# Optimization experiments

Hardware: AMD Instinct MI355X
Metric: run time of the kernel (lower is better)

The kernel has to match this reference:

```python
import jax, jax.numpy as jnp
import numpy as np

R, B, D, H, N, F = 8, 16, 32, 128, 2048, 256
HALF_LOG_2PI = np.float32(0.9189385332046727)  # 0.5*log(2*pi)


def _made_masks():
    # MADE masks for a 2-hidden-layer network (D -> H -> H -> 2*D), params=2,
    # input_order='random' per (region, batch) network, hidden degrees cyclic in [1, D-1].
    rng = np.random.RandomState(0)
    deg_in = np.stack([np.stack([rng.permutation(D) + 1 for _ in range(B)]) for _ in range(R)])  # [R,B,D]
    h_deg = (np.arange(H) % (D - 1)) + 1  # [H]
    M1 = (deg_in[:, :, :, None] <= h_deg[None, None, None, :]).astype(np.float32)  # [R,B,D,H]
    M2 = np.broadcast_to((h_deg[:, None] <= h_deg[None, :]).astype(np.float32), (R, B, H, H)).copy()  # [R,B,H,H]
    out_deg = np.repeat(deg_in, 2, axis=-1)  # [R,B,2D]; index k=2*d+p matches reshape(...,D,2)
    M3 = (h_deg[None, None, :, None] < out_deg[:, :, None, :]).astype(np.float32)  # [R,B,H,2D]
    return M1, M2, M3


def setup_inputs() -> dict:
    key = jax.random.key(0)
    k1, k2, k3, k4 = jax.random.split(key, 4)
    x = jax.random.normal(k1, (N, F), dtype=jnp.float32)
    W1 = jax.random.normal(k2, (R, B, D, H), dtype=jnp.float32) * 0.1
    W2 = jax.random.normal(k3, (R, B, H, H), dtype=jnp.float32) * 0.05
    W3 = jax.random.normal(k4, (R, B, H, 2 * D), dtype=jnp.float32) * 0.02
    M1, M2, M3 = _made_masks()
    region_idx = jnp.arange(F, dtype=jnp.int64 if jax.config.jax_enable_x64 else jnp.int32).reshape(R, D)
    return {"x": x, "W1": W1, "W2": W2, "W3": W3,
            "M1": jnp.asarray(M1), "M2": jnp.asarray(M2), "M3": jnp.asarray(M3),
            "region_idx": region_idx}


def reference(x, W1, W2, W3, M1, M2, M3, region_idx):
    # Gather per-region features: [N, R, D] -> [R, N, D]
    xr = jnp.transpose(x[:, region_idx], (1, 0, 2))
    # Masked MADE forward (no bias, relu), batched over all R*B networks.
    h1 = jax.nn.relu(jnp.einsum('rnd,rbdh->rbnh', xr, W1 * M1))
    h2 = jax.nn.relu(jnp.einsum('rbnh,rbhk->rbnk', h1, W2 * M2))
    out = jnp.einsum('rbnk,rbko->rbno', h2, W3 * M3)  # [R,B,N,2D]
    out = out.reshape(out.shape[0], out.shape[1], out.shape[2], -1, 2)  # [R,B,N,D,2]
    shift, log_scale = out[..., 0], out[..., 1]
    # MAF inverse (one pass): u = (y - shift) * exp(-log_scale);
    # log_prob = sum_d Normal(0,1).log_prob(u_d) - log_scale_d
    u = (xr[:, None] - shift) * jnp.exp(-log_scale)  # [R,B,N,D]
    ll = jnp.sum(-0.5 * u * u - HALF_LOG_2PI - log_scale, axis=-1)  # [R,B,N]
    return jnp.transpose(ll, (2, 0, 1))  # [N, R, B]
```

## Files before the change

### kernel.cpp

```cpp
#include <hip/hip_runtime.h>
#include <math.h>

constexpr int R_ = 8;
constexpr int B_ = 16;
constexpr int D_ = 32;
constexpr int H_ = 128;
constexpr int N_ = 2048;
constexpr int F_ = 256;
constexpr int O_ = 64;
constexpr float HLP_ = 0.9189385332046727f;

typedef float f32x4 __attribute__((ext_vector_type(4)));
typedef short bf16x8 __attribute__((ext_vector_type(8)));

__device__ __forceinline__ unsigned short f2bf(float f) {
    unsigned u = __builtin_bit_cast(unsigned, f);
    unsigned r = (u + 0x7FFFu + ((u >> 16) & 1u)) >> 16;
    return (unsigned short)r;
}

__device__ __forceinline__ int sl(int l) { return l ^ ((l >> 3) & 6); }

__global__ void pack_w(const float* __restrict__ W1, const float* __restrict__ M1,
                       const float* __restrict__ W2, const float* __restrict__ M2,
                       const float* __restrict__ W3, const float* __restrict__ M3,
                       unsigned short* __restrict__ P1, unsigned short* __restrict__ P2,
                       unsigned short* __restrict__ P3) {
    int gid  = blockIdx.x * blockDim.x + threadIdx.x;
    int lane = gid & 63;
    int frag = gid >> 6;
    if (frag >= 128 * 56) return;
    int rb  = frag / 56;
    int rem = frag - rb * 56;
    const float *W, *M;
    unsigned short* P;
    int K, Nn, kt, nt, fi;
    if (rem < 8)       { W = W1; M = M1; P = P1; K = 32;  Nn = 128; kt = 0;      nt = rem;   fi = rb * 8  + rem; }
    else if (rem < 40) { int q = rem - 8;  W = W2; M = M2; P = P2; K = 128; Nn = 128; kt = q >> 3; nt = q & 7; fi = rb * 32 + q; }
    else               { int q = rem - 40; W = W3; M = M3; P = P3; K = 128; Nn = 64;  kt = q >> 2; nt = q & 3; fi = rb * 16 + q; }
    int n  = nt * 16 + (lane & 15);
    int k0 = kt * 32 + ((lane >> 4) & 3) * 8;
    size_t src = (size_t)rb * K * Nn + (size_t)k0 * Nn + n;
    unsigned short v[8];
#pragma unroll
    for (int j = 0; j < 8; ++j)
        v[j] = f2bf(W[src + (size_t)j * Nn] * M[src + (size_t)j * Nn]);
    *(bf16x8*)(P + ((size_t)fi * 64 + lane) * 8) = *(bf16x8*)v;
}

__global__ __launch_bounds__(512, 4)
void flow_mfma(const float* __restrict__ x, const int* __restrict__ ridx,
               const unsigned short* __restrict__ P1,
               const unsigned short* __restrict__ P2,
               const unsigned short* __restrict__ P3,
               float* __restrict__ out)
{
    __shared__ __align__(16) unsigned short xbp[8 * 64 * 8];
    __shared__ __align__(16) unsigned short h1p[8 * 4 * 64 * 8];
    __shared__ __align__(16) unsigned short h2p[8 * 4 * 64 * 8];
    __shared__ float part[4][132];

    const int bid   = blockIdx.x;
    const int rb    = bid >> 4;
    const int chunk = bid & 15;
    const int n0    = chunk * 128;
    const int r     = rb >> 4;

    const int t    = threadIdx.x;
    const int lane = t & 63;
    const int w    = t >> 6;
    const int wm   = w & 1;
    const int wn   = w >> 1;
    const int q    = lane >> 4;
    const int c    = lane & 15;

    {
        int row = t >> 2;
        int dq  = t & 3;
        const int* rp = ridx + r * 32 + dq * 8;
        const float* xrow = x + (size_t)(n0 + row) * F_;
        unsigned short v[8];
#pragma unroll
        for (int j = 0; j < 8; ++j) v[j] = f2bf(xrow[rp[j]]);
        int mt = row >> 4;
        int lx = (row & 15) | (dq << 4);
        *(bf16x8*)&xbp[((mt * 64) + sl(lx)) * 8] = *(bf16x8*)v;
    }
    __syncthreads();

    {
        f32x4 acc1[4][2];
        bf16x8 af[4], bf_[2];
#pragma unroll
        for (int i = 0; i < 4; ++i) {
            int mt = wm * 4 + i;
            af[i] = *(bf16x8*)&xbp[(mt * 64 + sl(lane)) * 8];
        }
#pragma unroll
        for (int jn = 0; jn < 2; ++jn) {
            int nt = wn * 2 + jn;
            bf_[jn] = *(const bf16x8*)(P1 + ((size_t)(rb * 8 + nt) * 64 + lane) * 8);
        }
        f32x4 z = {0.f, 0.f, 0.f, 0.f};
#pragma unroll
        for (int i = 0; i < 4; ++i)
#pragma unroll
            for (int jn = 0; jn < 2; ++jn)
                acc1[i][jn] = __builtin_amdgcn_mfma_f32_16x16x32_bf16(af[i], bf_[jn], z, 0, 0, 0);
#pragma unroll
        for (int i = 0; i < 4; ++i) {
            int mt = wm * 4 + i;
#pragma unroll
            for (int jn = 0; jn < 2; ++jn) {
                int ntc   = wn * 2 + jn;
                int col   = ntc * 16 + c;
                int kt2   = col >> 5;
                int quad2 = (col >> 3) & 3;
                int j     = col & 7;
#pragma unroll
                for (int rg = 0; rg < 4; ++rg) {
                    float v = fmaxf(acc1[i][jn][rg], 0.f);
                    int l2 = (q * 4 + rg) | (quad2 << 4);
                    h1p[((mt * 4 + kt2) * 64 + sl(l2)) * 8 + j] = f2bf(v);
                }
            }
        }
    }
    __syncthreads();

    {
        f32x4 acc2[4][2];
#pragma unroll
        for (int i = 0; i < 4; ++i)
#pragma unroll
            for (int jn = 0; jn < 2; ++jn) acc2[i][jn] = (f32x4){0.f, 0.f, 0.f, 0.f};
#pragma unroll
        for (int kt = 0; kt < 4; ++kt) {
            bf16x8 bfr[2];
#pragma unroll
            for (int jn = 0; jn < 2; ++jn) {
                int nt = wn * 2 + jn;
                bfr[jn] = *(const bf16x8*)(P2 + ((size_t)(rb * 32 + kt * 8 + nt) * 64 + lane) * 8);
            }
#pragma unroll
            for (int i = 0; i < 4; ++i) {
                int mt = wm * 4 + i;
                bf16x8 a = *(bf16x8*)&h1p[((mt * 4 + kt) * 64 + sl(lane)) * 8];
#pragma unroll
                for (int jn = 0; jn < 2; ++jn)
                    acc2[i][jn] = __builtin_amdgcn_mfma_f32_16x16x32_bf16(a, bfr[jn], acc2[i][jn], 0, 0, 0);
            }
        }
#pragma unroll
        for (int i = 0; i < 4; ++i) {
            int mt = wm * 4 + i;
#pragma unroll
            for (int jn = 0; jn < 2; ++jn) {
                int ntc   = wn * 2 + jn;
                int col   = ntc * 16 + c;
                int kt2   = col >> 5;
                int quad2 = (col >> 3) & 3;
                int j     = col & 7;
#pragma unroll
                for (int rg = 0; rg < 4; ++rg) {
                    float v = fmaxf(acc2[i][jn][rg], 0.f);
                    int l2 = (q * 4 + rg) | (quad2 << 4);
                    h2p[((mt * 4 + kt2) * 64 + sl(l2)) * 8 + j] = f2bf(v);
                }
            }
        }
    }
    __syncthreads();

    {
        f32x4 acc3[4];
#pragma unroll
        for (int i = 0; i < 4; ++i) acc3[i] = (f32x4){0.f, 0.f, 0.f, 0.f};
#pragma unroll
        for (int kt = 0; kt < 4; ++kt) {
            bf16x8 b = *(const bf16x8*)(P3 + ((size_t)(rb * 16 + kt * 4 + wn) * 64 + lane) * 8);
#pragma unroll
            for (int i = 0; i < 4; ++i) {
                int mt = wm * 4 + i;
                bf16x8 a = *(bf16x8*)&h2p[((mt * 4 + kt) * 64 + sl(lane)) * 8];
                acc3[i] = __builtin_amdgcn_mfma_f32_16x16x32_bf16(a, b, acc3[i], 0, 0, 0);
            }
        }
        const int d    = wn * 8 + (c >> 1);
        const int colx = ridx[r * 32 + d];
        float xv[4][2];
#pragma unroll
        for (int i = 0; i < 4; ++i)
#pragma unroll
            for (int rr = 0; rr < 2; ++rr) {
                int rg  = (c & 1) * 2 + rr;
                int row = (wm * 4 + i) * 16 + q * 4 + rg;
                xv[i][rr] = x[(size_t)(n0 + row) * F_ + colx];
            }
        float ps[4][2];
#pragma unroll
        for (int i = 0; i < 4; ++i) {
            float oth[4];
#pragma unroll
            for (int rg = 0; rg < 4; ++rg) oth[rg] = __shfl_xor(acc3[i][rg], 1, 64);
#pragma unroll
            for (int rr = 0; rr < 2; ++rr) {
                int rg = (c & 1) * 2 + rr;
                float shift = (c & 1) ? oth[rg]     : acc3[i][rg];
                float ls    = (c & 1) ? acc3[i][rg] : oth[rg];
                float u = (xv[i][rr] - shift) * __expf(-ls);
                ps[i][rr] = fmaf(-0.5f * u, u, -HLP_ - ls);
            }
        }
#pragma unroll
        for (int m = 2; m <= 8; m <<= 1)
#pragma unroll
            for (int i = 0; i < 4; ++i) {
                ps[i][0] += __shfl_xor(ps[i][0], m, 64);
                ps[i][1] += __shfl_xor(ps[i][1], m, 64);
            }
        if ((c >> 1) == 0) {
#pragma unroll
            for (int i = 0; i < 4; ++i)
#pragma unroll
                for (int rr = 0; rr < 2; ++rr) {
                    int rg  = (c & 1) * 2 + rr;
                    int row = (wm * 4 + i) * 16 + q * 4 + rg;
                    part[wn][row] = ps[i][rr];
                }
        }
    }
    __syncthreads();

    if (t < 128) {
        float s = part[0][t] + part[1][t] + part[2][t] + part[3][t];
        out[(size_t)(n0 + t) * (R_ * B_) + rb] = s;
    }
}

__global__ __launch_bounds__(512, 2)
void flow_fb(const float* __restrict__ x,
             const float* __restrict__ W1, const float* __restrict__ W2,
             const float* __restrict__ W3,
             const float* __restrict__ M1, const float* __restrict__ M2,
             const float* __restrict__ M3,
             const int* __restrict__ ridx, float* __restrict__ out)
{
    __shared__ float xT[D_][132];
    __shared__ float h1T[H_][128];
    __shared__ float h2T[H_][128];
    __shared__ float part[16][132];
    const int bid = blockIdx.x, rb = bid >> 4, r = rb >> 4;
    const int n0 = (bid & 15) * 128;
    const int t = threadIdx.x, tr = t >> 4, tc = t & 15;
    const int tr4 = tr * 4, tc8 = tc * 8, tc4 = tc * 4;
    {
        int d = t & 31, rg = t >> 5;
        int col = ridx[r * D_ + d];
        const float* xp = x + (size_t)(n0 + rg * 8) * F_ + col;
#pragma unroll
        for (int i = 0; i < 8; ++i) xT[d][rg * 8 + i] = xp[i * F_];
    }
    __syncthreads();
    {
        float acc[4][8];
#pragma unroll
        for (int i = 0; i < 4; ++i)
#pragma unroll
            for (int j = 0; j < 8; ++j) acc[i][j] = 0.f;
        const float* Wb = W1 + (size_t)rb * D_ * H_;
        const float* Mb = M1 + (size_t)rb * D_ * H_;
        for (int k = 0; k < D_; ++k) {
            float a[4]; *(float4*)a = *(const float4*)&xT[k][tr4];
            const float* wr = Wb + k * H_ + tc8;
            const float* mr = Mb + k * H_ + tc8;
#pragma unroll
            for (int j = 0; j < 8; ++j) {
                float wv = wr[j] * mr[j];
#pragma unroll
                for (int i = 0; i < 4; ++i) acc[i][j] = fmaf(a[i], wv, acc[i][j]);
            }
        }
#pragma unroll
        for (int j = 0; j < 8; ++j) {
            float4 v = make_float4(fmaxf(acc[0][j], 0.f), fmaxf(acc[1][j], 0.f),
                                   fmaxf(acc[2][j], 0.f), fmaxf(acc[3][j], 0.f));
            *(float4*)&h1T[tc8 + j][tr4] = v;
        }
    }
    __syncthreads();
    {
        float acc[4][8];
#pragma unroll
        for (int i = 0; i < 4; ++i)
#pragma unroll
            for (int j = 0; j < 8; ++j) acc[i][j] = 0.f;
        const float* Wb = W2 + (size_t)rb * H_ * H_;
        const float* Mb = M2 + (size_t)rb * H_ * H_;
        for (int k = 0; k < H_; ++k) {
            float a[4]; *(float4*)a = *(const float4*)&h1T[k][tr4];
            const float* wr = Wb + k * H_ + tc8;
            const float* mr = Mb + k * H_ + tc8;
#pragma unroll
            for (int j = 0; j < 8; ++j) {
                float wv = wr[j] * mr[j];
#pragma unroll
                for (int i = 0; i < 4; ++i) acc[i][j] = fmaf(a[i], wv, acc[i][j]);
            }
        }
#pragma unroll
        for (int j = 0; j < 8; ++j) {
            float4 v = make_float4(fmaxf(acc[0][j], 0.f), fmaxf(acc[1][j], 0.f),
                                   fmaxf(acc[2][j], 0.f), fmaxf(acc[3][j], 0.f));
            *(float4*)&h2T[tc8 + j][tr4] = v;
        }
    }
    __syncthreads();
    {
        float acc[4][4];
#pragma unroll
        for (int i = 0; i < 4; ++i)
#pragma unroll
            for (int j = 0; j < 4; ++j) acc[i][j] = 0.f;
        const float* Wb = W3 + (size_t)rb * H_ * O_;
        const float* Mb = M3 + (size_t)rb * H_ * O_;
        for (int k = 0; k < H_; ++k) {
            float a[4]; *(float4*)a = *(const float4*)&h2T[k][tr4];
            const float* wr = Wb + k * O_ + tc4;
            const float* mr = Mb + k * O_ + tc4;
#pragma unroll
            for (int j = 0; j < 4; ++j) {
                float wv = wr[j] * mr[j];
#pragma unroll
                for (int i = 0; i < 4; ++i) acc[i][j] = fmaf(a[i], wv, acc[i][j]);
            }
        }
#pragma unroll
        for (int i = 0; i < 4; ++i) {
            int row = tr4 + i;
            float ll = 0.f;
#pragma unroll
            for (int qd = 0; qd < 2; ++qd) {
                float shift = acc[i][2 * qd], ls = acc[i][2 * qd + 1];
                float xvv = xT[2 * tc + qd][row];
                float u = (xvv - shift) * __expf(-ls);
                ll = fmaf(-0.5f * u, u, ll - HLP_ - ls);
            }
            part[tc][row] = ll;
        }
    }
    __syncthreads();
    if (t < 128) {
        float s = 0.f;
#pragma unroll
        for (int cc = 0; cc < 16; ++cc) s += part[cc][t];
        out[(size_t)(n0 + t) * (R_ * B_) + rb] = s;
    }
}

extern "C" void kernel_launch(void* const* d_in, const int* in_sizes, int n_in,
                              void* d_out, int out_size, void* d_ws, size_t ws_size,
                              hipStream_t stream) {
    const float* x   = (const float*)d_in[0];
    const float* W1  = (const float*)d_in[1];
    const float* W2  = (const float*)d_in[2];
    const float* W3  = (const float*)d_in[3];
    const float* M1  = (const float*)d_in[4];
    const float* M2  = (const float*)d_in[5];
    const float* M3  = (const float*)d_in[6];
    const int*  ridx = (const int*)d_in[7];
    float* out = (float*)d_out;

    const size_t s1 = (size_t)128 * 8  * 512;
    const size_t s2 = (size_t)128 * 32 * 512;
    const size_t s3 = (size_t)128 * 16 * 512;
    const size_t need = (s1 + s2 + s3) * sizeof(unsigned short);

    if (d_ws != nullptr && ws_size >= need) {
        unsigned short* P1 = (unsigned short*)d_ws;
        unsigned short* P2 = P1 + s1;
        unsigned short* P3 = P2 + s2;
        pack_w<<<dim3(1792), dim3(256), 0, stream>>>(W1, M1, W2, M2, W3, M3, P1, P2, P3);
        flow_mfma<<<dim3(2048), dim3(512), 0, stream>>>(x, ridx, P1, P2, P3, out);
    } else {
        flow_fb<<<dim3(2048), dim3(512), 0, stream>>>(x, W1, W2, W3, M1, M2, M3, ridx, out);
    }
}
```

Baseline: 133.0 us.

## Transpose MFMA operand roles, coalesce weight packing via LDS, prefetch weight fragments

The weight-packing kernel now reads W and M with coalesced float4 loads, stages them in a rotated LDS tile, and writes MFMA fragments from there, replacing strided scalar loads. The main kernel swaps GEMM operand roles so packed weights are the A operand (loaded straight into registers early and prefetched one k-step ahead), while activations become the B operand. It also writes h1/h2 with packed 64-bit stores and uses a cheaper round-to-nearest bf16 pack via perm. The epilogue is reorganized so each lane holds shift/log_scale pairs directly, which removes the xor-1 shuffle and shortens the reduction. Risks are higher register pressure from the prefetch and a slightly different bf16 rounding (ties are not rounded to even).

```diff
diff --git a/kernel.cpp b/kernel.cpp
--- a/kernel.cpp
+++ b/kernel.cpp
@@ -13,39 +13,66 @@
 typedef float f32x4 __attribute__((ext_vector_type(4)));
 typedef short bf16x8 __attribute__((ext_vector_type(8)));
 
-__device__ __forceinline__ unsigned short f2bf(float f) {
-    unsigned u = __builtin_bit_cast(unsigned, f);
-    unsigned r = (u + 0x7FFFu + ((u >> 16) & 1u)) >> 16;
-    return (unsigned short)r;
+__device__ __forceinline__ unsigned pk2(float lo, float hi) {
+    unsigned a = __builtin_bit_cast(unsigned, lo) + 0x8000u;
+    unsigned b = __builtin_bit_cast(unsigned, hi) + 0x8000u;
+    return __builtin_amdgcn_perm(b, a, 0x07060302);
 }
 
-__device__ __forceinline__ int sl(int l) { return l ^ ((l >> 3) & 6); }
-
-__global__ void pack_w(const float* __restrict__ W1, const float* __restrict__ M1,
-                       const float* __restrict__ W2, const float* __restrict__ M2,
-                       const float* __restrict__ W3, const float* __restrict__ M3,
-                       unsigned short* __restrict__ P1, unsigned short* __restrict__ P2,
-                       unsigned short* __restrict__ P3) {
-    int gid  = blockIdx.x * blockDim.x + threadIdx.x;
-    int lane = gid & 63;
-    int frag = gid >> 6;
-    if (frag >= 128 * 56) return;
-    int rb  = frag / 56;
-    int rem = frag - rb * 56;
-    const float *W, *M;
-    unsigned short* P;
-    int K, Nn, kt, nt, fi;
-    if (rem < 8)       { W = W1; M = M1; P = P1; K = 32;  Nn = 128; kt = 0;      nt = rem;   fi = rb * 8  + rem; }
-    else if (rem < 40) { int q = rem - 8;  W = W2; M = M2; P = P2; K = 128; Nn = 128; kt = q >> 3; nt = q & 7; fi = rb * 32 + q; }
-    else               { int q = rem - 40; W = W3; M = M3; P = P3; K = 128; Nn = 64;  kt = q >> 2; nt = q & 3; fi = rb * 16 + q; }
-    int n  = nt * 16 + (lane & 15);
-    int k0 = kt * 32 + ((lane >> 4) & 3) * 8;
-    size_t src = (size_t)rb * K * Nn + (size_t)k0 * Nn + n;
-    unsigned short v[8];
-#pragma unroll
-    for (int j = 0; j < 8; ++j)
-        v[j] = f2bf(W[src + (size_t)j * Nn] * M[src + (size_t)j * Nn]);
-    *(bf16x8*)(P + ((size_t)fi * 64 + lane) * 8) = *(bf16x8*)v;
+__global__ __launch_bounds__(256, 4)
+void pack_w(const float* __restrict__ W1, const float* __restrict__ M1,
+            const float* __restrict__ W2, const float* __restrict__ M2,
+            const float* __restrict__ W3, const float* __restrict__ M3,
+            unsigned short* __restrict__ P1, unsigned short* __restrict__ P2,
+            unsigned short* __restrict__ P3)
+{
+    __shared__ __align__(16) unsigned short tile[32 * 128];
+    const int bid = blockIdx.x;
+    const int t   = threadIdx.x;
+    const float *Wsrc, *Msrc;
+    unsigned short* dst;
+    int Mo, msh, frags;
+    if (bid < 128) {
+        int rb = bid;
+        Wsrc = W1 + (size_t)rb * 32 * 128;
+        Msrc = M1 + (size_t)rb * 32 * 128;
+        dst  = P1 + (size_t)rb * 8 * 512;
+        Mo = 128; msh = 7; frags = 8;
+    } else if (bid < 640) {
+        int s = bid - 128, rb = s >> 2, kt = s & 3;
+        Wsrc = W2 + (size_t)rb * 128 * 128 + (size_t)kt * 32 * 128;
+        Msrc = M2 + (size_t)rb * 128 * 128 + (size_t)kt * 32 * 128;
+        dst  = P2 + (size_t)(rb * 32 + kt * 8) * 512;
+        Mo = 128; msh = 7; frags = 8;
+    } else {
+        int s = bid - 640, rb = s >> 2, kt = s & 3;
+        Wsrc = W3 + (size_t)rb * 128 * 64 + (size_t)kt * 32 * 64;
+        Msrc = M3 + (size_t)rb * 128 * 64 + (size_t)kt * 32 * 64;
+        dst  = P3 + (size_t)(rb * 16 + kt * 4) * 512;
+        Mo = 64; msh = 6; frags = 4;
+    }
+    const int e4 = (32 << msh) >> 2;
+    for (int i = t; i < e4; i += 256) {
+        float4 wv = ((const float4*)Wsrc)[i];
+        float4 mv = ((const float4*)Msrc)[i];
+        unsigned lo = pk2(wv.x * mv.x, wv.y * mv.y);
+        unsigned hi = pk2(wv.z * mv.z, wv.w * mv.w);
+        int k = (i << 2) >> msh;
+        int m = (i << 2) & (Mo - 1);
+        int mr = (m + ((k >> 3) << 4)) & (Mo - 1);
+        *(uint2*)&tile[k * Mo + mr] = make_uint2(lo, hi);
+    }
+    __syncthreads();
+    const int no = frags * 64;
+    for (int o = t; o < no; o += 256) {
+        int mt = o >> 6, l = o & 63, cc = l & 15, qq = l >> 4;
+        unsigned short v[8];
+        int colr = ((mt * 16 + cc) + (qq << 4)) & (Mo - 1);
+#pragma unroll
+        for (int j = 0; j < 8; ++j)
+            v[j] = tile[(qq * 8 + j) * Mo + colr];
+        *(uint4*)(dst + (size_t)(mt * 64 + l) * 8) = *(uint4*)v;
+    }
 }
 
 __global__ __launch_bounds__(512, 4)
@@ -55,16 +82,15 @@
                const unsigned short* __restrict__ P3,
                float* __restrict__ out)
 {
-    __shared__ __align__(16) unsigned short xbp[8 * 64 * 8];
-    __shared__ __align__(16) unsigned short h1p[8 * 4 * 64 * 8];
-    __shared__ __align__(16) unsigned short h2p[8 * 4 * 64 * 8];
-    __shared__ float part[4][132];
-
-    const int bid   = blockIdx.x;
-    const int rb    = bid >> 4;
-    const int chunk = bid & 15;
-    const int n0    = chunk * 128;
-    const int r     = rb >> 4;
+    __shared__ __align__(16) unsigned short xB [8 * 64 * 8];
+    __shared__ __align__(16) unsigned short h1B[32 * 64 * 8];
+    __shared__ __align__(16) unsigned short h2B[32 * 64 * 8];
+    __shared__ float part[8][2][16];
+
+    const int bid = blockIdx.x;
+    const int rb  = bid >> 4;
+    const int n0  = (bid & 15) * 128;
+    const int r   = rb >> 4;
 
     const int t    = threadIdx.x;
     const int lane = t & 63;
@@ -74,166 +100,167 @@
     const int q    = lane >> 4;
     const int c    = lane & 15;
 
-    {
-        int row = t >> 2;
-        int dq  = t & 3;
+    bf16x8 a1[4];
+#pragma unroll
+    for (int i = 0; i < 4; ++i)
+        a1[i] = *(const bf16x8*)(P1 + ((size_t)(rb * 8 + wm * 4 + i) * 64 + lane) * 8);
+
+    {
+        int nl = t >> 2;
+        int dq = t & 3;
         const int* rp = ridx + r * 32 + dq * 8;
-        const float* xrow = x + (size_t)(n0 + row) * F_;
-        unsigned short v[8];
-#pragma unroll
-        for (int j = 0; j < 8; ++j) v[j] = f2bf(xrow[rp[j]]);
-        int mt = row >> 4;
-        int lx = (row & 15) | (dq << 4);
-        *(bf16x8*)&xbp[((mt * 64) + sl(lx)) * 8] = *(bf16x8*)v;
-    }
-    __syncthreads();
-
-    {
-        f32x4 acc1[4][2];
-        bf16x8 af[4], bf_[2];
+        int cols[8];
+#pragma unroll
+        for (int j = 0; j < 8; ++j) cols[j] = rp[j];
+        const float* xrow = x + (size_t)(n0 + nl) * F_;
+        unsigned pk[4];
+#pragma unroll
+        for (int j = 0; j < 4; ++j)
+            pk[j] = pk2(xrow[cols[2 * j]], xrow[cols[2 * j + 1]]);
+        int slot = ((nl >> 4) * 64) + (dq << 4) + (nl & 15);
+        *(uint4*)&xB[slot * 8] = make_uint4(pk[0], pk[1], pk[2], pk[3]);
+    }
+    __syncthreads();
+
+    {
+        bf16x8 b1[2];
+#pragma unroll
+        for (int jn = 0; jn < 2; ++jn)
+            b1[jn] = *(bf16x8*)&xB[((wn * 2 + jn) * 64 + lane) * 8];
+        f32x4 z = {0.f, 0.f, 0.f, 0.f};
+        f32x4 acc[4][2];
+#pragma unroll
+        for (int i = 0; i < 4; ++i)
+#pragma unroll
+            for (int jn = 0; jn < 2; ++jn)
+                acc[i][jn] = __builtin_amdgcn_mfma_f32_16x16x32_bf16(a1[i], b1[jn], z, 0, 0, 0);
 #pragma unroll
         for (int i = 0; i < 4; ++i) {
-            int mt = wm * 4 + i;
-            af[i] = *(bf16x8*)&xbp[(mt * 64 + sl(lane)) * 8];
-        }
+            int mt  = wm * 4 + i;
+            int ktw = mt >> 1;
+            int qw  = (2 * mt + (q >> 1)) & 3;
+            int j0h = (q & 1) * 4;
+#pragma unroll
+            for (int jn = 0; jn < 2; ++jn) {
+                int nt = wn * 2 + jn;
+                unsigned lo = pk2(fmaxf(acc[i][jn][0], 0.f), fmaxf(acc[i][jn][1], 0.f));
+                unsigned hi = pk2(fmaxf(acc[i][jn][2], 0.f), fmaxf(acc[i][jn][3], 0.f));
+                *(uint2*)&h1B[(((nt * 4 + ktw) * 64) + qw * 16 + c) * 8 + j0h] = make_uint2(lo, hi);
+            }
+        }
+    }
+    bf16x8 a2[4];
+#pragma unroll
+    for (int i = 0; i < 4; ++i)
+        a2[i] = *(const bf16x8*)(P2 + ((size_t)(rb * 32 + wm * 4 + i) * 64 + lane) * 8);
+    __syncthreads();
+
+    f32x4 acc2[4][2];
+#pragma unroll
+    for (int i = 0; i < 4; ++i)
+#pragma unroll
+        for (int jn = 0; jn < 2; ++jn) acc2[i][jn] = (f32x4){0.f, 0.f, 0.f, 0.f};
+#pragma unroll
+    for (int kt = 0; kt < 4; ++kt) {
+        bf16x8 bb[2];
+#pragma unroll
+        for (int jn = 0; jn < 2; ++jn)
+            bb[jn] = *(bf16x8*)&h1B[(((wn * 2 + jn) * 4 + kt) * 64 + lane) * 8];
+        bf16x8 an[4];
+        if (kt < 3) {
+#pragma unroll
+            for (int i = 0; i < 4; ++i)
+                an[i] = *(const bf16x8*)(P2 + ((size_t)(rb * 32 + (kt + 1) * 8 + wm * 4 + i) * 64 + lane) * 8);
+        }
+#pragma unroll
+        for (int i = 0; i < 4; ++i)
+#pragma unroll
+            for (int jn = 0; jn < 2; ++jn)
+                acc2[i][jn] = __builtin_amdgcn_mfma_f32_16x16x32_bf16(a2[i], bb[jn], acc2[i][jn], 0, 0, 0);
+        if (kt < 3) {
+#pragma unroll
+            for (int i = 0; i < 4; ++i) a2[i] = an[i];
+        }
+    }
+    bf16x8 a3[2];
+#pragma unroll
+    for (int im = 0; im < 2; ++im)
+        a3[im] = *(const bf16x8*)(P3 + ((size_t)(rb * 16 + wm * 2 + im) * 64 + lane) * 8);
+#pragma unroll
+    for (int i = 0; i < 4; ++i) {
+        int mt  = wm * 4 + i;
+        int ktw = mt >> 1;
+        int qw  = (2 * mt + (q >> 1)) & 3;
+        int j0h = (q & 1) * 4;
 #pragma unroll
         for (int jn = 0; jn < 2; ++jn) {
             int nt = wn * 2 + jn;
-            bf_[jn] = *(const bf16x8*)(P1 + ((size_t)(rb * 8 + nt) * 64 + lane) * 8);
-        }
-        f32x4 z = {0.f, 0.f, 0.f, 0.f};
-#pragma unroll
-        for (int i = 0; i < 4; ++i)
+            unsigned lo = pk2(fmaxf(acc2[i][jn][0], 0.f), fmaxf(acc2[i][jn][1], 0.f));
+            unsigned hi = pk2(fmaxf(acc2[i][jn][2], 0.f), fmaxf(acc2[i][jn][3], 0.f));
+            *(uint2*)&h2B[(((nt * 4 + ktw) * 64) + qw * 16 + c) * 8 + j0h] = make_uint2(lo, hi);
+        }
+    }
+    __syncthreads();
+
+    {
+        f32x4 acc3[2][2];
+#pragma unroll
+        for (int im = 0; im < 2; ++im)
+#pragma unroll
+            for (int jn = 0; jn < 2; ++jn) acc3[im][jn] = (f32x4){0.f, 0.f, 0.f, 0.f};
+#pragma unroll
+        for (int kt = 0; kt < 4; ++kt) {
+            bf16x8 bb[2];
 #pragma unroll
             for (int jn = 0; jn < 2; ++jn)
-                acc1[i][jn] = __builtin_amdgcn_mfma_f32_16x16x32_bf16(af[i], bf_[jn], z, 0, 0, 0);
-#pragma unroll
-        for (int i = 0; i < 4; ++i) {
-            int mt = wm * 4 + i;
+                bb[jn] = *(bf16x8*)&h2B[(((wn * 2 + jn) * 4 + kt) * 64 + lane) * 8];
+            bf16x8 an[2];
+            if (kt < 3) {
+#pragma unroll
+                for (int im = 0; im < 2; ++im)
+                    an[im] = *(const bf16x8*)(P3 + ((size_t)(rb * 16 + (kt + 1) * 4 + wm * 2 + im) * 64 + lane) * 8);
+            }
+#pragma unroll
+            for (int im = 0; im < 2; ++im)
+#pragma unroll
+                for (int jn = 0; jn < 2; ++jn)
+                    acc3[im][jn] = __builtin_amdgcn_mfma_f32_16x16x32_bf16(a3[im], bb[jn], acc3[im][jn], 0, 0, 0);
+            if (kt < 3) { a3[0] = an[0]; a3[1] = an[1]; }
+        }
+        float pll[2] = {0.f, 0.f};
+#pragma unroll
+        for (int im = 0; im < 2; ++im) {
+            int mt3 = wm * 2 + im;
+            int d0  = mt3 * 8 + q * 2;
+            int col0 = ridx[r * 32 + d0];
+            int col1 = ridx[r * 32 + d0 + 1];
 #pragma unroll
             for (int jn = 0; jn < 2; ++jn) {
-                int ntc   = wn * 2 + jn;
-                int col   = ntc * 16 + c;
-                int kt2   = col >> 5;
-                int quad2 = (col >> 3) & 3;
-                int j     = col & 7;
-#pragma unroll
-                for (int rg = 0; rg < 4; ++rg) {
-                    float v = fmaxf(acc1[i][jn][rg], 0.f);
-                    int l2 = (q * 4 + rg) | (quad2 << 4);
-                    h1p[((mt * 4 + kt2) * 64 + sl(l2)) * 8 + j] = f2bf(v);
-                }
-            }
-        }
-    }
-    __syncthreads();
-
-    {
-        f32x4 acc2[4][2];
-#pragma unroll
-        for (int i = 0; i < 4; ++i)
-#pragma unroll
-            for (int jn = 0; jn < 2; ++jn) acc2[i][jn] = (f32x4){0.f, 0.f, 0.f, 0.f};
-#pragma unroll
-        for (int kt = 0; kt < 4; ++kt) {
-            bf16x8 bfr[2];
-#pragma unroll
-            for (int jn = 0; jn < 2; ++jn) {
-                int nt = wn * 2 + jn;
-                bfr[jn] = *(const bf16x8*)(P2 + ((size_t)(rb * 32 + kt * 8 + nt) * 64 + lane) * 8);
-            }
-#pragma unroll
-            for (int i = 0; i < 4; ++i) {
-                int mt = wm * 4 + i;
-                bf16x8 a = *(bf16x8*)&h1p[((mt * 4 + kt) * 64 + sl(lane)) * 8];
-#pragma unroll
-                for (int jn = 0; jn < 2; ++jn)
-                    acc2[i][jn] = __builtin_amdgcn_mfma_f32_16x16x32_bf16(a, bfr[jn], acc2[i][jn], 0, 0, 0);
-            }
-        }
-#pragma unroll
-        for (int i = 0; i < 4; ++i) {
-            int mt = wm * 4 + i;
-#pragma unroll
-            for (int jn = 0; jn < 2; ++jn) {
-                int ntc   = wn * 2 + jn;
-                int col   = ntc * 16 + c;
-                int kt2   = col >> 5;
-                int quad2 = (col >> 3) & 3;
-                int j     = col & 7;
-#pragma unroll
-                for (int rg = 0; rg < 4; ++rg) {
-                    float v = fmaxf(acc2[i][jn][rg], 0.f);
-                    int l2 = (q * 4 + rg) | (quad2 << 4);
-                    h2p[((mt * 4 + kt2) * 64 + sl(l2)) * 8 + j] = f2bf(v);
-                }
-            }
-        }
-    }
-    __syncthreads();
-
-    {
-        f32x4 acc3[4];
-#pragma unroll
-        for (int i = 0; i < 4; ++i) acc3[i] = (f32x4){0.f, 0.f, 0.f, 0.f};
-#pragma unroll
-        for (int kt = 0; kt < 4; ++kt) {
-            bf16x8 b = *(const bf16x8*)(P3 + ((size_t)(rb * 16 + kt * 4 + wn) * 64 + lane) * 8);
-#pragma unroll
-            for (int i = 0; i < 4; ++i) {
-                int mt = wm * 4 + i;
-                bf16x8 a = *(bf16x8*)&h2p[((mt * 4 + kt) * 64 + sl(lane)) * 8];
-                acc3[i] = __builtin_amdgcn_mfma_f32_16x16x32_bf16(a, b, acc3[i], 0, 0, 0);
-            }
-        }
-        const int d    = wn * 8 + (c >> 1);
-        const int colx = ridx[r * 32 + d];
-        float xv[4][2];
-#pragma unroll
-        for (int i = 0; i < 4; ++i)
-#pragma unroll
-            for (int rr = 0; rr < 2; ++rr) {
-                int rg  = (c & 1) * 2 + rr;
-                int row = (wm * 4 + i) * 16 + q * 4 + rg;
-                xv[i][rr] = x[(size_t)(n0 + row) * F_ + colx];
-            }
-        float ps[4][2];
-#pragma unroll
-        for (int i = 0; i < 4; ++i) {
-            float oth[4];
-#pragma unroll
-            for (int rg = 0; rg < 4; ++rg) oth[rg] = __shfl_xor(acc3[i][rg], 1, 64);
-#pragma unroll
-            for (int rr = 0; rr < 2; ++rr) {
-                int rg = (c & 1) * 2 + rr;
-                float shift = (c & 1) ? oth[rg]     : acc3[i][rg];
-                float ls    = (c & 1) ? acc3[i][rg] : oth[rg];
-                float u = (xv[i][rr] - shift) * __expf(-ls);
-                ps[i][rr] = fmaf(-0.5f * u, u, -HLP_ - ls);
-            }
-        }
-#pragma unroll
-        for (int m = 2; m <= 8; m <<= 1)
-#pragma unroll
-            for (int i = 0; i < 4; ++i) {
-                ps[i][0] += __shfl_xor(ps[i][0], m, 64);
-                ps[i][1] += __shfl_xor(ps[i][1], m, 64);
-            }
-        if ((c >> 1) == 0) {
-#pragma unroll
-            for (int i = 0; i < 4; ++i)
-#pragma unroll
-                for (int rr = 0; rr < 2; ++rr) {
-                    int rg  = (c & 1) * 2 + rr;
-                    int row = (wm * 4 + i) * 16 + q * 4 + rg;
-                    part[wn][row] = ps[i][rr];
-                }
+                int n = n0 + (wn * 2 + jn) * 16 + c;
+                const float* xr_ = x + (size_t)n * F_;
+                float x0 = xr_[col0], x1 = xr_[col1];
+                float sh0 = acc3[im][jn][0], ls0 = acc3[im][jn][1];
+                float sh1 = acc3[im][jn][2], ls1 = acc3[im][jn][3];
+                float u0 = (x0 - sh0) * __expf(-ls0);
+                float u1 = (x1 - sh1) * __expf(-ls1);
+                pll[jn] += fmaf(-0.5f * u0, u0, -HLP_ - ls0) + fmaf(-0.5f * u1, u1, -HLP_ - ls1);
+            }
+        }
+#pragma unroll
+        for (int jn = 0; jn < 2; ++jn) {
+            pll[jn] += __shfl_xor(pll[jn], 16, 64);
+            pll[jn] += __shfl_xor(pll[jn], 32, 64);
+        }
+        if (q == 0) {
+            part[w][0][c] = pll[0];
+            part[w][1][c] = pll[1];
         }
     }
     __syncthreads();
 
     if (t < 128) {
-        float s = part[0][t] + part[1][t] + part[2][t] + part[3][t];
+        int wnf = t >> 5, jnf = (t >> 4) & 1, cf = t & 15;
+        float s = part[wnf * 2 + 0][jnf][cf] + part[wnf * 2 + 1][jnf][cf];
         out[(size_t)(n0 + t) * (R_ * B_) + rb] = s;
     }
 }
@@ -380,7 +407,7 @@
         unsigned short* P1 = (unsigned short*)d_ws;
         unsigned short* P2 = P1 + s1;
         unsigned short* P3 = P2 + s2;
-        pack_w<<<dim3(1792), dim3(256), 0, stream>>>(W1, M1, W2, M2, W3, M3, P1, P2, P3);
+        pack_w<<<dim3(1152), dim3(256), 0, stream>>>(W1, M1, W2, M2, W3, M3, P1, P2, P3);
         flow_mfma<<<dim3(2048), dim3(512), 0, stream>>>(x, ridx, P1, P2, P3, out);
     } else {
         flow_fb<<<dim3(2048), dim3(512), 0, stream>>>(x, W1, W2, W3, M1, M2, M3, ridx, out);
```

New measurement: 136.8 us. 2.8% more time.
